# Performance work log

Measured on AMD Instinct MI355X. Metric: run time of the kernel, lower is better.

Reference implementation:

```python
import jax, jax.numpy as jnp
import numpy as np

NUM_HEADS = 8
GROUP_SIZE = 4
INF = 1000000.0


def _group(x, mask, g):
    # x: [N, L, D] -> [N, L//g, D] (mean over group); mask: any over group
    N, L, D = x.shape
    xg = x.reshape(N, L // g, g, D).mean(axis=2)
    mg = mask.reshape(N, L // g, g).any(axis=2)
    return xg, mg


def _heads(x, h):
    N, L, D = x.shape
    return x.reshape(N, L, h, D // h)


def _alpha(logits, mask_row, mask_col):
    # logits: [N, L1, L2, H]; masks: [N, L1], [N, L2] (same across heads)
    pair = (mask_row[:, :, None] & mask_col[:, None, :])[..., None]  # [N,L1,L2,1]
    logits = jnp.where(pair, logits, logits - INF)
    alpha = jax.nn.softmax(logits, axis=2)
    return jnp.where(mask_row[:, :, None, None], alpha, jnp.zeros_like(alpha))


def setup_inputs() -> dict:
    key = jax.random.key(0)
    ks = jax.random.split(key, 9)
    N, Lp, Ls, D = 32, 4096, 1024, 256
    protein = jax.random.normal(ks[0], (N, Lp, D), dtype=jnp.float32)
    sm = jax.random.normal(ks[1], (N, Ls, D), dtype=jnp.float32)
    mask_prot = jax.random.randint(ks[2], (N, Lp), 0, 2) > 0
    mask_sm = jax.random.randint(ks[3], (N, Ls), 0, 2) > 0
    scale = 1.0 / np.sqrt(D)
    Wk_p = jax.random.normal(ks[4], (D, D), dtype=jnp.float32) * scale
    Wv_p = jax.random.normal(ks[5], (D, D), dtype=jnp.float32) * scale
    Wq_d = jax.random.normal(ks[6], (D, D), dtype=jnp.float32) * scale
    Wk_d = jax.random.normal(ks[7], (D, D), dtype=jnp.float32) * scale
    Wv_d = jax.random.normal(ks[8], (D, D), dtype=jnp.float32) * scale
    return {"protein": protein, "sm": sm, "mask_prot": mask_prot,
            "mask_sm": mask_sm, "Wk_p": Wk_p, "Wv_p": Wv_p,
            "Wq_d": Wq_d, "Wk_d": Wk_d, "Wv_d": Wv_d}


def reference(protein, sm, mask_prot, mask_sm, Wk_p, Wv_p, Wq_d, Wk_d, Wv_d):
    H = NUM_HEADS
    prot_g, mprot_g = _group(protein, mask_prot, GROUP_SIZE)
    sm_g, msm_g = _group(sm, mask_sm, GROUP_SIZE)

    key_prot = _heads(prot_g @ Wk_p, H)   # [N, Gp, H, d]
    val_prot = _heads(prot_g @ Wv_p, H)
    query_sm = _heads(sm_g @ Wq_d, H)     # [N, Gs, H, d]
    key_sm = _heads(sm_g @ Wk_d, H)
    val_sm = _heads(sm_g @ Wv_d, H)

    logits_dp = jnp.einsum('blhd,bkhd->blkh', query_sm, key_prot)
    logits_dd = jnp.einsum('blhd,bkhd->blkh', query_sm, key_sm)

    alpha_dp = _alpha(logits_dp, msm_g, mprot_g)
    alpha_dd = _alpha(logits_dd, msm_g, msm_g)

    out_dp = jnp.einsum('blkh,bkhd->blhd', alpha_dp, val_prot)
    out_dd = jnp.einsum('blkh,bkhd->blhd', alpha_dd, val_sm)
    N, Gs = out_dp.shape[0], out_dp.shape[1]
    return (out_dp.reshape(N, Gs, -1) + out_dd.reshape(N, Gs, -1)) * 0.5
```

## Files before the change

### kernel.cpp

```cpp
#include <hip/hip_runtime.h>
#include <cstdint>
#include <cstddef>

#define N_B 32
#define D_MODEL 256
#define H_N 8
#define HD 32
#define GP 1024
#define GS 256
#define LOG2E 1.4426950408889634f

typedef __attribute__((ext_vector_type(8))) short short8;
typedef __attribute__((ext_vector_type(4))) float floatx4;

#if __has_builtin(__builtin_amdgcn_exp2f)
#define EXP2(x) __builtin_amdgcn_exp2f(x)
#else
#define EXP2(x) exp2f(x)
#endif

__device__ __forceinline__ unsigned short f2bf(float f) {
    unsigned u = __float_as_uint(f);
    u = (u + 0x7FFFu + ((u >> 16) & 1u)) >> 16;
    return (unsigned short)u;
}

__device__ __forceinline__ unsigned pack_bf16(float a, float b) {
    unsigned ua = __float_as_uint(a) + 0x8000u;
    unsigned ub = __float_as_uint(b) + 0x8000u;
    return __builtin_amdgcn_perm(ub, ua, 0x07060302);
}

__global__ void group_mean_bf16(const float4* __restrict__ x,
                                ushort4* __restrict__ xg, int total) {
    int gid = blockIdx.x * blockDim.x + threadIdx.x;
    if (gid >= total) return;
    int row = gid >> 6;
    int c   = gid & 63;
    const float4* p = x + (size_t)row * 256 + c;
    float4 a = p[0], b = p[64], cc = p[128], d = p[192];
    ushort4 r;
    r.x = f2bf(0.25f * (a.x + b.x + cc.x + d.x));
    r.y = f2bf(0.25f * (a.y + b.y + cc.y + d.y));
    r.z = f2bf(0.25f * (a.z + b.z + cc.z + d.z));
    r.w = f2bf(0.25f * (a.w + b.w + cc.w + d.w));
    xg[gid] = r;
}

__global__ void group_mask_bias(const int* __restrict__ m,
                                float* __restrict__ bias, int total) {
    int gid = blockIdx.x * blockDim.x + threadIdx.x;
    if (gid >= total) return;
    const int* p = m + (size_t)gid * 4;
    bias[gid] = (p[0] | p[1] | p[2] | p[3]) ? 0.0f : -1442695.0f;
}

__global__ __launch_bounds__(256) void wtrans_bf16(
        const float* __restrict__ W0, const float* __restrict__ W1,
        const float* __restrict__ W2, unsigned short* __restrict__ WT) {
    __shared__ unsigned short sT[64 * 65];
    int p = blockIdx.y;
    int kt = blockIdx.x >> 2, ct = blockIdx.x & 3;
    const float* W = (p == 0) ? W0 : (p == 1 ? W1 : W2);
    int k0 = kt * 64, c0 = ct * 64;
    int t = threadIdx.x;
#pragma unroll
    for (int j = 0; j < 4; j++) {
        int idx = j * 256 + t;
        int kr = idx >> 4, cf = idx & 15;
        float4 v = *(const float4*)&W[(size_t)(k0 + kr) * 256 + c0 + cf * 4];
        sT[(cf * 4 + 0) * 65 + kr] = f2bf(v.x);
        sT[(cf * 4 + 1) * 65 + kr] = f2bf(v.y);
        sT[(cf * 4 + 2) * 65 + kr] = f2bf(v.z);
        sT[(cf * 4 + 3) * 65 + kr] = f2bf(v.w);
    }
    __syncthreads();
#pragma unroll
    for (int j = 0; j < 8; j++) {
        int idx = j * 256 + t;
        int cw = idx >> 5, kq = idx & 31;
        unsigned lo = sT[cw * 65 + kq * 2];
        unsigned hi = sT[cw * 65 + kq * 2 + 1];
        ((unsigned*)WT)[((size_t)p * 256 + c0 + cw) * 128 + (k0 >> 1) + kq] =
            lo | (hi << 16);
    }
}

__global__ __launch_bounds__(256) void vtrans(
        const unsigned short* __restrict__ V, unsigned short* __restrict__ Vt,
        int Gk) {
    __shared__ unsigned short sT[32 * 132];
    int nh = blockIdx.y, kbase = blockIdx.x << 7;
    const uint4* src = (const uint4*)(V + ((size_t)nh * Gk + kbase) * 32);
    int t = threadIdx.x;
#pragma unroll
    for (int j = 0; j < 2; j++) {
        int idx = j * 256 + t;
        int kk = idx >> 2, dq = idx & 3;
        union { uint4 u; unsigned short s[8]; } w;
        w.u = src[kk * 4 + dq];
#pragma unroll
        for (int e = 0; e < 8; e++)
            sT[(dq * 8 + e) * 132 + kk] = w.s[e];
    }
    __syncthreads();
#pragma unroll
    for (int j = 0; j < 2; j++) {
        int idx = j * 256 + t;
        int d = idx >> 4, pu = idx & 15;
        union { uint4 u; unsigned short s[8]; } w;
#pragma unroll
        for (int e = 0; e < 8; e++) {
            int p = pu * 8 + e;
            int chunk = p >> 5, p32 = p & 31;
            int k32 = (p32 >> 1) + ((p32 & 1) << 4);
            w.s[e] = sT[d * 132 + chunk * 32 + k32];
        }
        *(uint4*)(Vt + ((size_t)nh * 32 + d) * Gk + kbase + pu * 8) = w.u;
    }
}

__global__ __launch_bounds__(256) void gemm_bf16(
        const unsigned short* __restrict__ A,
        const unsigned short* __restrict__ WT,
        unsigned short* __restrict__ o0, unsigned short* __restrict__ o1,
        unsigned short* __restrict__ o2, int Gg, int lgG, float scale0) {
    __shared__ alignas(16) unsigned short As[128 * 64];
    __shared__ alignas(16) unsigned short Bs[128 * 64];
    const int tid = threadIdx.x;
    const int ln = tid & 63, wave = tid >> 6;
    const int m16 = ln & 15, quad = ln >> 4;
    const int wm = (wave & 1) * 64, wn = (wave >> 1) * 64;
    const int row0 = blockIdx.y * 128, col0 = blockIdx.x * 128;

    const uint4* gA[4];
    const uint4* gB[4];
    unsigned ldsoff[4];
#pragma unroll
    for (int j = 0; j < 4; j++) {
        int u = (j * 4 + wave) * 64 + ln;
        int r = u >> 3, s = u & 7;
        int sg = (s - r) & 7;
        gA[j] = (const uint4*)A + (size_t)(row0 + r) * 32 + sg;
        gB[j] = (const uint4*)WT + (size_t)(col0 + r) * 32 + sg;
        ldsoff[j] = (unsigned)((j * 4 + wave) * 512);
    }
    int aaddr[4], baddr[4];
#pragma unroll
    for (int i = 0; i < 4; i++) {
        int rA = wm + i * 16 + m16;
        aaddr[i] = rA * 128 + ((quad + rA) & 7) * 16;
        int rB = wn + i * 16 + m16;
        baddr[i] = rB * 128 + ((quad + rB) & 7) * 16;
    }

    floatx4 acc[4][4] = {};
    for (int ko = 0; ko < 32; ko += 8) {
        __syncthreads();
#pragma unroll
        for (int j = 0; j < 4; j++) {
            __builtin_amdgcn_global_load_lds(
                (const __attribute__((address_space(1))) void*)(gA[j] + ko),
                (__attribute__((address_space(3))) void*)&As[ldsoff[j]], 16, 0, 0);
            __builtin_amdgcn_global_load_lds(
                (const __attribute__((address_space(1))) void*)(gB[j] + ko),
                (__attribute__((address_space(3))) void*)&Bs[ldsoff[j]], 16, 0, 0);
        }
        __syncthreads();
#pragma unroll
        for (int kh = 0; kh < 2; kh++) {
            short8 af[4], bfr[4];
#pragma unroll
            for (int i = 0; i < 4; i++) {
                af[i]  = *(const short8*)((const char*)As + (aaddr[i] ^ (kh << 6)));
                bfr[i] = *(const short8*)((const char*)Bs + (baddr[i] ^ (kh << 6)));
            }
#pragma unroll
            for (int im = 0; im < 4; im++)
#pragma unroll
                for (int in = 0; in < 4; in++)
                    acc[im][in] = __builtin_amdgcn_mfma_f32_16x16x32_bf16(
                        af[im], bfr[in], acc[im][in], 0, 0, 0);
        }
    }
#pragma unroll
    for (int im = 0; im < 4; im++) {
#pragma unroll
        for (int in = 0; in < 4; in++) {
            int colg = col0 + wn + in * 16 + m16;
            int p = colg >> 8, h = (colg >> 5) & 7, d = colg & 31;
            unsigned short* ob = (p == 0) ? o0 : (p == 1 ? o1 : o2);
            float sc = (p == 0) ? scale0 : 1.0f;
#pragma unroll
            for (int r = 0; r < 4; r++) {
                int Mrow = row0 + wm + im * 16 + quad * 4 + r;
                int nb = Mrow >> lgG, g = Mrow & (Gg - 1);
                ob[(((size_t)nb * 8 + h) * Gg + g) * 32 + d] = f2bf(acc[im][in][r] * sc);
            }
        }
    }
}

__device__ __forceinline__ void attn_stream(
        const unsigned short* __restrict__ Kb,
        const unsigned short* __restrict__ Vtb,
        const float* __restrict__ bias, int Lk, short8 qf, unsigned* sPw,
        int m16, int quad, float* l, floatx4& o0, floatx4& o1) {
    const uint4* K4 = (const uint4*)Kb;
    const uint4* V4 = (const uint4*)Vtb;
    const int Gk8 = Lk >> 3;
    const int nchunks = Lk >> 5;
    for (int c = 0; c < nchunks; c++) {
        union { uint4 u; short8 v; } kf0, kf1, vf0, vf1, pf;
        kf0.u = K4[(c * 32 + m16) * 4 + quad];
        kf1.u = K4[(c * 32 + 16 + m16) * 4 + quad];
        vf0.u = V4[(size_t)m16 * Gk8 + c * 4 + quad];
        vf1.u = V4[(size_t)(16 + m16) * Gk8 + c * 4 + quad];
        floatx4 z = {0.f, 0.f, 0.f, 0.f};
        floatx4 s0 = __builtin_amdgcn_mfma_f32_16x16x32_bf16(qf, kf0.v, z, 0, 0, 0);
        floatx4 s1 = __builtin_amdgcn_mfma_f32_16x16x32_bf16(qf, kf1.v, z, 0, 0, 0);
        float b0 = bias[c * 32 + m16];
        float b1 = bias[c * 32 + 16 + m16];
#pragma unroll
        for (int r = 0; r < 4; r++) {
            float e0 = EXP2(s0[r] + b0);
            float e1 = EXP2(s1[r] + b1);
            l[r] += e0 + e1;
            sPw[(quad * 4 + r) * 20 + m16] = pack_bf16(e0, e1);
        }
        pf.u = *(const uint4*)&sPw[m16 * 20 + quad * 4];
        o0 = __builtin_amdgcn_mfma_f32_16x16x32_bf16(pf.v, vf0.v, o0, 0, 0, 0);
        o1 = __builtin_amdgcn_mfma_f32_16x16x32_bf16(pf.v, vf1.v, o1, 0, 0, 0);
    }
}

__global__ __launch_bounds__(256) void attn_mfma(
        const unsigned short* __restrict__ Qd, const unsigned short* __restrict__ Kp,
        const unsigned short* __restrict__ Vpt, const unsigned short* __restrict__ Ksd,
        const unsigned short* __restrict__ Vsdt, const float* __restrict__ bias_p,
        const float* __restrict__ bias_s, float* __restrict__ out) {
    __shared__ alignas(16) unsigned sP[4][16 * 20];
    const int b = blockIdx.x;
    const int n = b >> 5, h = (b >> 2) & 7, qq = b & 3;
    const int tid = threadIdx.x, wave = tid >> 6, ln = tid & 63;
    const int m16 = ln & 15, quad = ln >> 4;
    const int q0 = qq * 64 + wave * 16;
    unsigned* sPw = sP[wave];

    union { uint4 u; short8 v; } qf;
    qf.u = ((const uint4*)Qd)[(((size_t)n * 8 + h) * GS + q0 + m16) * 4 + quad];

    float l_dp[4] = {0, 0, 0, 0}, l_dd[4] = {0, 0, 0, 0};
    floatx4 odp0 = {}, odp1 = {}, odd0 = {}, odd1 = {};

    attn_stream(Kp + ((size_t)n * 8 + h) * GP * 32,
                Vpt + ((size_t)n * 8 + h) * GP * 32,
                bias_p + (size_t)n * GP, GP, qf.v, sPw, m16, quad,
                l_dp, odp0, odp1);
    attn_stream(Ksd + ((size_t)n * 8 + h) * GS * 32,
                Vsdt + ((size_t)n * 8 + h) * GS * 32,
                bias_s + (size_t)n * GS, GS, qf.v, sPw, m16, quad,
                l_dd, odd0, odd1);

#pragma unroll
    for (int r = 0; r < 4; r++) {
#pragma unroll
        for (int off = 1; off < 16; off <<= 1) {
            l_dp[r] += __shfl_xor(l_dp[r], off, 64);
            l_dd[r] += __shfl_xor(l_dd[r], off, 64);
        }
    }
#pragma unroll
    for (int r = 0; r < 4; r++) {
        int qrow = q0 + quad * 4 + r;
        bool rm = (bias_s[(size_t)n * GS + qrow] == 0.0f);
        float idp = 1.f / l_dp[r], idd = 1.f / l_dd[r];
        float v0 = rm ? 0.5f * (odp0[r] * idp + odd0[r] * idd) : 0.f;
        float v1 = rm ? 0.5f * (odp1[r] * idp + odd1[r] * idd) : 0.f;
        float* ob = out + ((size_t)n * GS + qrow) * 256 + h * 32;
        ob[m16] = v0;
        ob[16 + m16] = v1;
    }
}

extern "C" void kernel_launch(void* const* d_in, const int* in_sizes, int n_in,
                              void* d_out, int out_size, void* d_ws,
                              size_t ws_size, hipStream_t stream) {
    const float* protein   = (const float*)d_in[0];
    const float* smx       = (const float*)d_in[1];
    const int*   mask_prot = (const int*)d_in[2];
    const int*   mask_sm   = (const int*)d_in[3];
    const float* Wk_p = (const float*)d_in[4];
    const float* Wv_p = (const float*)d_in[5];
    const float* Wq_d = (const float*)d_in[6];
    const float* Wk_d = (const float*)d_in[7];
    const float* Wv_d = (const float*)d_in[8];
    float* out = (float*)d_out;

    char* ws = (char*)d_ws;
    unsigned short* prot_g = (unsigned short*)ws; ws += (size_t)N_B * GP * 256 * 2;
    unsigned short* sm_g   = (unsigned short*)ws; ws += (size_t)N_B * GS * 256 * 2;
    unsigned short* WTbig  = (unsigned short*)ws; ws += (size_t)512 * 256 * 2;
    unsigned short* WTsml  = (unsigned short*)ws; ws += (size_t)768 * 256 * 2;
    unsigned short* Kp     = (unsigned short*)ws; ws += (size_t)N_B * H_N * GP * 32 * 2;
    unsigned short* Vp     = (unsigned short*)ws; ws += (size_t)N_B * H_N * GP * 32 * 2;
    unsigned short* Vpt    = (unsigned short*)ws; ws += (size_t)N_B * H_N * GP * 32 * 2;
    unsigned short* Qd     = (unsigned short*)ws; ws += (size_t)N_B * H_N * GS * 32 * 2;
    unsigned short* Ksd    = (unsigned short*)ws; ws += (size_t)N_B * H_N * GS * 32 * 2;
    unsigned short* Vsd    = (unsigned short*)ws; ws += (size_t)N_B * H_N * GS * 32 * 2;
    unsigned short* Vsdt   = (unsigned short*)ws; ws += (size_t)N_B * H_N * GS * 32 * 2;
    float* bias_p = (float*)ws; ws += (size_t)N_B * GP * 4;
    float* bias_s = (float*)ws; ws += (size_t)N_B * GS * 4;

    int totalP = N_B * GP * 64;
    group_mean_bf16<<<totalP / 256, 256, 0, stream>>>(
        (const float4*)protein, (ushort4*)prot_g, totalP);
    int totalS = N_B * GS * 64;
    group_mean_bf16<<<totalS / 256, 256, 0, stream>>>(
        (const float4*)smx, (ushort4*)sm_g, totalS);
    group_mask_bias<<<(N_B * GP) / 256, 256, 0, stream>>>(
        mask_prot, bias_p, N_B * GP);
    group_mask_bias<<<(N_B * GS) / 256, 256, 0, stream>>>(
        mask_sm, bias_s, N_B * GS);

    wtrans_bf16<<<dim3(16, 2), 256, 0, stream>>>(Wk_p, Wv_p, Wv_p, WTbig);
    wtrans_bf16<<<dim3(16, 3), 256, 0, stream>>>(Wq_d, Wk_d, Wv_d, WTsml);

    gemm_bf16<<<dim3(4, (N_B * GP) / 128), 256, 0, stream>>>(
        prot_g, WTbig, Kp, Vp, Vp, GP, 10, 1.0f);
    gemm_bf16<<<dim3(6, (N_B * GS) / 128), 256, 0, stream>>>(
        sm_g, WTsml, Qd, Ksd, Vsd, GS, 8, LOG2E);

    vtrans<<<dim3(GP / 128, N_B * H_N), 256, 0, stream>>>(Vp, Vpt, GP);
    vtrans<<<dim3(GS / 128, N_B * H_N), 256, 0, stream>>>(Vsd, Vsdt, GS);

    attn_mfma<<<N_B * H_N * 4, 256, 0, stream>>>(Qd, Kp, Vpt, Ksd, Vsdt,
                                                 bias_p, bias_s, out);
}
```

Before: 329.9 us.

## Merge launch pairs and give each attention wave two query tiles with prefetch

Each pair of same-shaped launches (group mean, mask bias, weight transpose, projection GEMM, V transpose) is merged into a single launch that branches on block index, which cuts the number of kernel launches. The attention kernel now has each wave handle 32 query rows as two 16-row MFMA tiles, so every K/V fragment loaded is reused twice. K/V/bias fragments for the next chunk are also loaded before the current chunk is computed, to hide global load latency. In exchange, the attention grid is halved to 512 blocks and register use rises, which may lower occupancy.

Result: faster. 293.8 us (-10.9%).

```diff
diff --git a/kernel.cpp b/kernel.cpp
--- a/kernel.cpp
+++ b/kernel.cpp
@@ -31,37 +31,54 @@
     return __builtin_amdgcn_perm(ub, ua, 0x07060302);
 }
 
-__global__ void group_mean_bf16(const float4* __restrict__ x,
-                                ushort4* __restrict__ xg, int total) {
-    int gid = blockIdx.x * blockDim.x + threadIdx.x;
-    if (gid >= total) return;
-    int row = gid >> 6;
-    int c   = gid & 63;
-    const float4* p = x + (size_t)row * 256 + c;
-    float4 a = p[0], b = p[64], cc = p[128], d = p[192];
-    ushort4 r;
-    r.x = f2bf(0.25f * (a.x + b.x + cc.x + d.x));
-    r.y = f2bf(0.25f * (a.y + b.y + cc.y + d.y));
-    r.z = f2bf(0.25f * (a.z + b.z + cc.z + d.z));
-    r.w = f2bf(0.25f * (a.w + b.w + cc.w + d.w));
-    xg[gid] = r;
-}
-
-__global__ void group_mask_bias(const int* __restrict__ m,
-                                float* __restrict__ bias, int total) {
-    int gid = blockIdx.x * blockDim.x + threadIdx.x;
-    if (gid >= total) return;
-    const int* p = m + (size_t)gid * 4;
-    bias[gid] = (p[0] | p[1] | p[2] | p[3]) ? 0.0f : -1442695.0f;
+#define PRO_A (N_B * GP * 64)
+#define PRO_B (N_B * GS * 64)
+#define PRO_C (N_B * GP)
+#define PRO_D (N_B * GS)
+__global__ __launch_bounds__(256) void prologue(
+        const float4* __restrict__ prot, const float4* __restrict__ smx,
+        const int* __restrict__ mp, const int* __restrict__ ms,
+        ushort4* __restrict__ prot_g, ushort4* __restrict__ sm_g,
+        float* __restrict__ bias_p, float* __restrict__ bias_s) {
+    int gid = blockIdx.x * 256 + threadIdx.x;
+    if (gid < PRO_A + PRO_B) {
+        const float4* x; ushort4* xg; int g2;
+        if (gid < PRO_A) { x = prot; xg = prot_g; g2 = gid; }
+        else { x = smx; xg = sm_g; g2 = gid - PRO_A; }
+        int row = g2 >> 6, c = g2 & 63;
+        const float4* p = x + (size_t)row * 256 + c;
+        float4 a = p[0], b = p[64], cc = p[128], d = p[192];
+        ushort4 r;
+        r.x = f2bf(0.25f * (a.x + b.x + cc.x + d.x));
+        r.y = f2bf(0.25f * (a.y + b.y + cc.y + d.y));
+        r.z = f2bf(0.25f * (a.z + b.z + cc.z + d.z));
+        r.w = f2bf(0.25f * (a.w + b.w + cc.w + d.w));
+        xg[g2] = r;
+    } else {
+        int g2 = gid - (PRO_A + PRO_B);
+        const int* m; float* bias;
+        if (g2 < PRO_C) { m = mp; bias = bias_p; }
+        else { m = ms; bias = bias_s; g2 -= PRO_C; }
+        const int* p = m + (size_t)g2 * 4;
+        bias[g2] = (p[0] | p[1] | p[2] | p[3]) ? 0.0f : -1442695.0f;
+    }
 }
 
 __global__ __launch_bounds__(256) void wtrans_bf16(
-        const float* __restrict__ W0, const float* __restrict__ W1,
-        const float* __restrict__ W2, unsigned short* __restrict__ WT) {
+        const float* __restrict__ Wk_p, const float* __restrict__ Wv_p,
+        const float* __restrict__ Wq_d, const float* __restrict__ Wk_d,
+        const float* __restrict__ Wv_d,
+        unsigned short* __restrict__ WTbig, unsigned short* __restrict__ WTsml) {
     __shared__ unsigned short sT[64 * 65];
-    int p = blockIdx.y;
+    int y = blockIdx.y;
+    const float* W; unsigned short* WT; int pidx;
+    if (y < 2) { W = (y == 0) ? Wk_p : Wv_p; WT = WTbig; pidx = y; }
+    else {
+        int q = y - 2;
+        W = (q == 0) ? Wq_d : (q == 1 ? Wk_d : Wv_d);
+        WT = WTsml; pidx = q;
+    }
     int kt = blockIdx.x >> 2, ct = blockIdx.x & 3;
-    const float* W = (p == 0) ? W0 : (p == 1 ? W1 : W2);
     int k0 = kt * 64, c0 = ct * 64;
     int t = threadIdx.x;
 #pragma unroll
@@ -81,16 +98,19 @@
         int cw = idx >> 5, kq = idx & 31;
         unsigned lo = sT[cw * 65 + kq * 2];
         unsigned hi = sT[cw * 65 + kq * 2 + 1];
-        ((unsigned*)WT)[((size_t)p * 256 + c0 + cw) * 128 + (k0 >> 1) + kq] =
+        ((unsigned*)WT)[((size_t)pidx * 256 + c0 + cw) * 128 + (k0 >> 1) + kq] =
             lo | (hi << 16);
     }
 }
 
 __global__ __launch_bounds__(256) void vtrans(
-        const unsigned short* __restrict__ V, unsigned short* __restrict__ Vt,
-        int Gk) {
+        const unsigned short* __restrict__ Vp, unsigned short* __restrict__ Vpt,
+        const unsigned short* __restrict__ Vs, unsigned short* __restrict__ Vst) {
     __shared__ unsigned short sT[32 * 132];
-    int nh = blockIdx.y, kbase = blockIdx.x << 7;
+    int nh = blockIdx.y, bx = blockIdx.x;
+    const unsigned short* V; unsigned short* Vt; int Gk, kbase;
+    if (bx < 8) { V = Vp; Vt = Vpt; Gk = GP; kbase = bx << 7; }
+    else { V = Vs; Vt = Vst; Gk = GS; kbase = (bx - 8) << 7; }
     const uint4* src = (const uint4*)(V + ((size_t)nh * Gk + kbase) * 32);
     int t = threadIdx.x;
 #pragma unroll
@@ -121,17 +141,34 @@
 }
 
 __global__ __launch_bounds__(256) void gemm_bf16(
-        const unsigned short* __restrict__ A,
-        const unsigned short* __restrict__ WT,
-        unsigned short* __restrict__ o0, unsigned short* __restrict__ o1,
-        unsigned short* __restrict__ o2, int Gg, int lgG, float scale0) {
+        const unsigned short* __restrict__ Abig,
+        const unsigned short* __restrict__ WTbig,
+        const unsigned short* __restrict__ Asml,
+        const unsigned short* __restrict__ WTsml,
+        unsigned short* __restrict__ Kp, unsigned short* __restrict__ Vp,
+        unsigned short* __restrict__ Qd, unsigned short* __restrict__ Ksd,
+        unsigned short* __restrict__ Vsd) {
     __shared__ alignas(16) unsigned short As[128 * 64];
     __shared__ alignas(16) unsigned short Bs[128 * 64];
+    int id = blockIdx.x;
+    const unsigned short *A, *WT;
+    unsigned short *o0, *o1, *o2;
+    int Gg, lgG, row0, col0;
+    float scale0;
+    if (id < 1024) {
+        A = Abig; WT = WTbig; o0 = Kp; o1 = Vp; o2 = Vp;
+        Gg = GP; lgG = 10; scale0 = 1.0f;
+        col0 = (id & 3) << 7; row0 = (id >> 2) << 7;
+    } else {
+        int t = id - 1024;
+        A = Asml; WT = WTsml; o0 = Qd; o1 = Ksd; o2 = Vsd;
+        Gg = GS; lgG = 8; scale0 = LOG2E;
+        col0 = (t % 6) << 7; row0 = (t / 6) << 7;
+    }
     const int tid = threadIdx.x;
     const int ln = tid & 63, wave = tid >> 6;
     const int m16 = ln & 15, quad = ln >> 4;
     const int wm = (wave & 1) * 64, wn = (wave >> 1) * 64;
-    const int row0 = blockIdx.y * 128, col0 = blockIdx.x * 128;
 
     const uint4* gA[4];
     const uint4* gB[4];
@@ -201,36 +238,62 @@
     }
 }
 
+struct KVFrag { uint4 k0, k1, v0, v1; float b0, b1; };
+
+__device__ __forceinline__ KVFrag load_frag(
+        const uint4* K4, const uint4* V4, const float* bias,
+        int c, int Gk8, int m16, int quad) {
+    KVFrag f;
+    f.k0 = K4[(c * 32 + m16) * 4 + quad];
+    f.k1 = K4[(c * 32 + 16 + m16) * 4 + quad];
+    f.v0 = V4[(size_t)m16 * Gk8 + c * 4 + quad];
+    f.v1 = V4[(size_t)(16 + m16) * Gk8 + c * 4 + quad];
+    f.b0 = bias[c * 32 + m16];
+    f.b1 = bias[c * 32 + 16 + m16];
+    return f;
+}
+
 __device__ __forceinline__ void attn_stream(
         const unsigned short* __restrict__ Kb,
         const unsigned short* __restrict__ Vtb,
-        const float* __restrict__ bias, int Lk, short8 qf, unsigned* sPw,
-        int m16, int quad, float* l, floatx4& o0, floatx4& o1) {
+        const float* __restrict__ bias, int Lk,
+        short8 qfA, short8 qfB, unsigned* sPw,
+        int m16, int quad, float* lA, float* lB,
+        floatx4& oA0, floatx4& oA1, floatx4& oB0, floatx4& oB1) {
     const uint4* K4 = (const uint4*)Kb;
     const uint4* V4 = (const uint4*)Vtb;
     const int Gk8 = Lk >> 3;
     const int nchunks = Lk >> 5;
+    KVFrag cur = load_frag(K4, V4, bias, 0, Gk8, m16, quad);
     for (int c = 0; c < nchunks; c++) {
-        union { uint4 u; short8 v; } kf0, kf1, vf0, vf1, pf;
-        kf0.u = K4[(c * 32 + m16) * 4 + quad];
-        kf1.u = K4[(c * 32 + 16 + m16) * 4 + quad];
-        vf0.u = V4[(size_t)m16 * Gk8 + c * 4 + quad];
-        vf1.u = V4[(size_t)(16 + m16) * Gk8 + c * 4 + quad];
+        int cn = (c + 1 < nchunks) ? c + 1 : c;
+        KVFrag nxt = load_frag(K4, V4, bias, cn, Gk8, m16, quad);
+        union { uint4 u; short8 v; } t0, t1, pA, pB;
+        t0.u = cur.k0; t1.u = cur.k1;
         floatx4 z = {0.f, 0.f, 0.f, 0.f};
-        floatx4 s0 = __builtin_amdgcn_mfma_f32_16x16x32_bf16(qf, kf0.v, z, 0, 0, 0);
-        floatx4 s1 = __builtin_amdgcn_mfma_f32_16x16x32_bf16(qf, kf1.v, z, 0, 0, 0);
-        float b0 = bias[c * 32 + m16];
-        float b1 = bias[c * 32 + 16 + m16];
+        floatx4 sA0 = __builtin_amdgcn_mfma_f32_16x16x32_bf16(qfA, t0.v, z, 0, 0, 0);
+        floatx4 sA1 = __builtin_amdgcn_mfma_f32_16x16x32_bf16(qfA, t1.v, z, 0, 0, 0);
+        floatx4 sB0 = __builtin_amdgcn_mfma_f32_16x16x32_bf16(qfB, t0.v, z, 0, 0, 0);
+        floatx4 sB1 = __builtin_amdgcn_mfma_f32_16x16x32_bf16(qfB, t1.v, z, 0, 0, 0);
 #pragma unroll
         for (int r = 0; r < 4; r++) {
-            float e0 = EXP2(s0[r] + b0);
-            float e1 = EXP2(s1[r] + b1);
-            l[r] += e0 + e1;
-            sPw[(quad * 4 + r) * 20 + m16] = pack_bf16(e0, e1);
-        }
-        pf.u = *(const uint4*)&sPw[m16 * 20 + quad * 4];
-        o0 = __builtin_amdgcn_mfma_f32_16x16x32_bf16(pf.v, vf0.v, o0, 0, 0, 0);
-        o1 = __builtin_amdgcn_mfma_f32_16x16x32_bf16(pf.v, vf1.v, o1, 0, 0, 0);
+            float eA0 = EXP2(sA0[r] + cur.b0);
+            float eA1 = EXP2(sA1[r] + cur.b1);
+            float eB0 = EXP2(sB0[r] + cur.b0);
+            float eB1 = EXP2(sB1[r] + cur.b1);
+            lA[r] += eA0 + eA1;
+            lB[r] += eB0 + eB1;
+            sPw[(quad * 4 + r) * 20 + m16] = pack_bf16(eA0, eA1);
+            sPw[320 + (quad * 4 + r) * 20 + m16] = pack_bf16(eB0, eB1);
+        }
+        pA.u = *(const uint4*)&sPw[m16 * 20 + quad * 4];
+        pB.u = *(const uint4*)&sPw[320 + m16 * 20 + quad * 4];
+        t0.u = cur.v0; t1.u = cur.v1;
+        oA0 = __builtin_amdgcn_mfma_f32_16x16x32_bf16(pA.v, t0.v, oA0, 0, 0, 0);
+        oA1 = __builtin_amdgcn_mfma_f32_16x16x32_bf16(pA.v, t1.v, oA1, 0, 0, 0);
+        oB0 = __builtin_amdgcn_mfma_f32_16x16x32_bf16(pB.v, t0.v, oB0, 0, 0, 0);
+        oB1 = __builtin_amdgcn_mfma_f32_16x16x32_bf16(pB.v, t1.v, oB1, 0, 0, 0);
+        cur = nxt;
     }
 }
 
@@ -239,47 +302,56 @@
         const unsigned short* __restrict__ Vpt, const unsigned short* __restrict__ Ksd,
         const unsigned short* __restrict__ Vsdt, const float* __restrict__ bias_p,
         const float* __restrict__ bias_s, float* __restrict__ out) {
-    __shared__ alignas(16) unsigned sP[4][16 * 20];
+    __shared__ alignas(16) unsigned sP[4][640];
     const int b = blockIdx.x;
-    const int n = b >> 5, h = (b >> 2) & 7, qq = b & 3;
+    const int n = b >> 4, h = (b >> 1) & 7, qq = b & 1;
     const int tid = threadIdx.x, wave = tid >> 6, ln = tid & 63;
     const int m16 = ln & 15, quad = ln >> 4;
-    const int q0 = qq * 64 + wave * 16;
+    const int q0 = qq * 128 + wave * 32;
     unsigned* sPw = sP[wave];
 
-    union { uint4 u; short8 v; } qf;
-    qf.u = ((const uint4*)Qd)[(((size_t)n * 8 + h) * GS + q0 + m16) * 4 + quad];
-
-    float l_dp[4] = {0, 0, 0, 0}, l_dd[4] = {0, 0, 0, 0};
-    floatx4 odp0 = {}, odp1 = {}, odd0 = {}, odd1 = {};
+    union { uint4 u; short8 v; } qfA, qfB;
+    qfA.u = ((const uint4*)Qd)[(((size_t)n * 8 + h) * GS + q0 + m16) * 4 + quad];
+    qfB.u = ((const uint4*)Qd)[(((size_t)n * 8 + h) * GS + q0 + 16 + m16) * 4 + quad];
+
+    float lAdp[4] = {0, 0, 0, 0}, lBdp[4] = {0, 0, 0, 0};
+    float lAdd[4] = {0, 0, 0, 0}, lBdd[4] = {0, 0, 0, 0};
+    floatx4 oAdp0 = {}, oAdp1 = {}, oBdp0 = {}, oBdp1 = {};
+    floatx4 oAdd0 = {}, oAdd1 = {}, oBdd0 = {}, oBdd1 = {};
 
     attn_stream(Kp + ((size_t)n * 8 + h) * GP * 32,
                 Vpt + ((size_t)n * 8 + h) * GP * 32,
-                bias_p + (size_t)n * GP, GP, qf.v, sPw, m16, quad,
-                l_dp, odp0, odp1);
+                bias_p + (size_t)n * GP, GP, qfA.v, qfB.v, sPw, m16, quad,
+                lAdp, lBdp, oAdp0, oAdp1, oBdp0, oBdp1);
     attn_stream(Ksd + ((size_t)n * 8 + h) * GS * 32,
                 Vsdt + ((size_t)n * 8 + h) * GS * 32,
-                bias_s + (size_t)n * GS, GS, qf.v, sPw, m16, quad,
-                l_dd, odd0, odd1);
+                bias_s + (size_t)n * GS, GS, qfA.v, qfB.v, sPw, m16, quad,
+                lAdd, lBdd, oAdd0, oAdd1, oBdd0, oBdd1);
 
 #pragma unroll
     for (int r = 0; r < 4; r++) {
 #pragma unroll
         for (int off = 1; off < 16; off <<= 1) {
-            l_dp[r] += __shfl_xor(l_dp[r], off, 64);
-            l_dd[r] += __shfl_xor(l_dd[r], off, 64);
+            lAdp[r] += __shfl_xor(lAdp[r], off, 64);
+            lBdp[r] += __shfl_xor(lBdp[r], off, 64);
+            lAdd[r] += __shfl_xor(lAdd[r], off, 64);
+            lBdd[r] += __shfl_xor(lBdd[r], off, 64);
         }
     }
 #pragma unroll
     for (int r = 0; r < 4; r++) {
-        int qrow = q0 + quad * 4 + r;
-        bool rm = (bias_s[(size_t)n * GS + qrow] == 0.0f);
-        float idp = 1.f / l_dp[r], idd = 1.f / l_dd[r];
-        float v0 = rm ? 0.5f * (odp0[r] * idp + odd0[r] * idd) : 0.f;
-        float v1 = rm ? 0.5f * (odp1[r] * idp + odd1[r] * idd) : 0.f;
-        float* ob = out + ((size_t)n * GS + qrow) * 256 + h * 32;
-        ob[m16] = v0;
-        ob[16 + m16] = v1;
+        int qrowA = q0 + quad * 4 + r;
+        bool rmA = (bias_s[(size_t)n * GS + qrowA] == 0.0f);
+        float idpA = 1.f / lAdp[r], iddA = 1.f / lAdd[r];
+        float* obA = out + ((size_t)n * GS + qrowA) * 256 + h * 32;
+        obA[m16]      = rmA ? 0.5f * (oAdp0[r] * idpA + oAdd0[r] * iddA) : 0.f;
+        obA[16 + m16] = rmA ? 0.5f * (oAdp1[r] * idpA + oAdd1[r] * iddA) : 0.f;
+        int qrowB = q0 + 16 + quad * 4 + r;
+        bool rmB = (bias_s[(size_t)n * GS + qrowB] == 0.0f);
+        float idpB = 1.f / lBdp[r], iddB = 1.f / lBdd[r];
+        float* obB = out + ((size_t)n * GS + qrowB) * 256 + h * 32;
+        obB[m16]      = rmB ? 0.5f * (oBdp0[r] * idpB + oBdd0[r] * iddB) : 0.f;
+        obB[16 + m16] = rmB ? 0.5f * (oBdp1[r] * idpB + oBdd1[r] * iddB) : 0.f;
     }
 }
 
@@ -312,28 +384,18 @@
     float* bias_p = (float*)ws; ws += (size_t)N_B * GP * 4;
     float* bias_s = (float*)ws; ws += (size_t)N_B * GS * 4;
 
-    int totalP = N_B * GP * 64;
-    group_mean_bf16<<<totalP / 256, 256, 0, stream>>>(
-        (const float4*)protein, (ushort4*)prot_g, totalP);
-    int totalS = N_B * GS * 64;
-    group_mean_bf16<<<totalS / 256, 256, 0, stream>>>(
-        (const float4*)smx, (ushort4*)sm_g, totalS);
-    group_mask_bias<<<(N_B * GP) / 256, 256, 0, stream>>>(
-        mask_prot, bias_p, N_B * GP);
-    group_mask_bias<<<(N_B * GS) / 256, 256, 0, stream>>>(
-        mask_sm, bias_s, N_B * GS);
-
-    wtrans_bf16<<<dim3(16, 2), 256, 0, stream>>>(Wk_p, Wv_p, Wv_p, WTbig);
-    wtrans_bf16<<<dim3(16, 3), 256, 0, stream>>>(Wq_d, Wk_d, Wv_d, WTsml);
-
-    gemm_bf16<<<dim3(4, (N_B * GP) / 128), 256, 0, stream>>>(
-        prot_g, WTbig, Kp, Vp, Vp, GP, 10, 1.0f);
-    gemm_bf16<<<dim3(6, (N_B * GS) / 128), 256, 0, stream>>>(
-        sm_g, WTsml, Qd, Ksd, Vsd, GS, 8, LOG2E);
-
-    vtrans<<<dim3(GP / 128, N_B * H_N), 256, 0, stream>>>(Vp, Vpt, GP);
-    vtrans<<<dim3(GS / 128, N_B * H_N), 256, 0, stream>>>(Vsd, Vsdt, GS);
-
-    attn_mfma<<<N_B * H_N * 4, 256, 0, stream>>>(Qd, Kp, Vpt, Ksd, Vsdt,
+    prologue<<<(PRO_A + PRO_B + PRO_C + PRO_D) / 256, 256, 0, stream>>>(
+        (const float4*)protein, (const float4*)smx, mask_prot, mask_sm,
+        (ushort4*)prot_g, (ushort4*)sm_g, bias_p, bias_s);
+
+    wtrans_bf16<<<dim3(16, 5), 256, 0, stream>>>(
+        Wk_p, Wv_p, Wq_d, Wk_d, Wv_d, WTbig, WTsml);
+
+    gemm_bf16<<<1024 + 384, 256, 0, stream>>>(
+        prot_g, WTbig, sm_g, WTsml, Kp, Vp, Qd, Ksd, Vsd);
+
+    vtrans<<<dim3(10, N_B * H_N), 256, 0, stream>>>(Vp, Vpt, Vsd, Vsdt);
+
+    attn_mfma<<<N_B * H_N * 2, 256, 0, stream>>>(Qd, Kp, Vpt, Ksd, Vsdt,
                                                  bias_p, bias_s, out);
 }
```
